# Performance work log

Hardware: AMD Instinct MI355X
Metric: run time of the kernel (lower is better)

The kernel has to match this reference:

```python
import jax, jax.numpy as jnp
import numpy as np

N6 = 100000
N8 = 100000
E = 400000
D = 128


def setup_inputs() -> dict:
    key = jax.random.key(0)
    ks = jax.random.split(key, 12)
    def msg(k):
        return jax.random.normal(k, (E, D), dtype=jnp.float32)
    def W(k):
        return jax.random.normal(k, (D, D), dtype=jnp.float32) / np.sqrt(D)
    def ei(k, n):
        return jax.random.randint(k, (E, 2), 0, n, dtype=jnp.int32)
    return {
        "msg_66": msg(ks[0]), "msg_68": msg(ks[1]),
        "msg_86": msg(ks[2]), "msg_88": msg(ks[3]),
        "W_66": W(ks[4]), "W_68": W(ks[5]), "W_86": W(ks[6]), "W_88": W(ks[7]),
        "ei_66": ei(ks[8], N6), "ei_68": ei(ks[9], N8),
        "ei_86": ei(ks[10], N6), "ei_88": ei(ks[11], N8),
        "num_nodes_6": N6, "num_nodes_8": N8,
    }


def _scatter_mean(v, dst, num_nodes):
    # torch_scatter reduce='mean': sum / count, count clamped to >=1 (zeros stay zero)
    s = jax.ops.segment_sum(v, dst, num_segments=num_nodes)
    c = jax.ops.segment_sum(jnp.ones((dst.shape[0],), v.dtype), dst, num_segments=num_nodes)
    return s / jnp.maximum(c, 1.0)[:, None]


def _proj_scatter(msg, W, ei, num_nodes):
    # per-edge-type linear (bias=False) then scatter-mean to dst nodes
    out = _scatter_mean(msg @ W, ei[:, 1], num_nodes)          # (num_nodes, D)
    # non-zero-row indicator (computed on detached values in the original)
    mask = jnp.any(jax.lax.stop_gradient(out) != 0, axis=-1).astype(out.dtype)  # (num_nodes,)
    return out, mask


def reference(msg_66, msg_68, msg_86, msg_88,
              W_66, W_68, W_86, W_88,
              ei_66, ei_68, ei_86, ei_88,
              num_nodes_6, num_nodes_8):
    # dict iteration order: "6-6", "6-8", "8-6", "8-8"; dst type is last token of key
    o66, m66 = _proj_scatter(msg_66, W_66, ei_66, num_nodes_6)
    o68, m68 = _proj_scatter(msg_68, W_68, ei_68, num_nodes_8)
    o86, m86 = _proj_scatter(msg_86, W_86, ei_86, num_nodes_6)
    o88, m88 = _proj_scatter(msg_88, W_88, ei_88, num_nodes_8)
    out_6 = jnp.stack([o66, o86], axis=1)   # (N6, num_edge_types_to_6=2, D)
    out_8 = jnp.stack([o68, o88], axis=1)   # (N8, 2, D)
    num_types_6 = m66 + m86                 # (N6,)
    num_types_8 = m68 + m88                 # (N8,)
    return out_6, out_8, num_types_6, num_types_8
```

## Files before the change

### kernel.cpp

```cpp
#include <hip/hip_runtime.h>

#define DF    128
#define EPB   1024
#define MAXB  512
#define TPB   64
#define ATS   132
#define WSTS  136
#define CAP   512

typedef __attribute__((ext_vector_type(8))) short short8;
typedef __attribute__((ext_vector_type(4))) float f32x4;

__device__ __forceinline__ unsigned short f2bf(float x) {
    unsigned u = __float_as_uint(x);
    u = (u + 0x7FFFu + ((u >> 16) & 1u)) >> 16;
    return (unsigned short)u;
}
__device__ __forceinline__ unsigned pack2bf(float a, float b) {
    return (unsigned)f2bf(a) | ((unsigned)f2bf(b) << 16);
}
__device__ __forceinline__ int rfl(int x) {
    return __builtin_amdgcn_readfirstlane(x);
}

struct AllParams {
    const float* msg[4];
    const float* Wm[4];
    float*       outp[4];
    int gb[4];
    int eb[4];
    int N[4];
    int cum[5];
};


__global__ void __launch_bounds__(256) count_kernel(
    const int* __restrict__ ei66, const int* __restrict__ ei86,
    const int* __restrict__ ei68, const int* __restrict__ ei88,
    int E66, int E86, int E68, int E88, int N6, int N8,
    int* __restrict__ base)
{
    int Etot = E66 + E86 + E68 + E88;
    for (int gid = blockIdx.x * 256 + threadIdx.x; gid < Etot;
         gid += gridDim.x * 256) {
        int le = gid, nb, dst;
        if (le < E66)               { dst = ei66[2 * le + 1]; nb = 0; }
        else if ((le -= E66) < E86) { dst = ei86[2 * le + 1]; nb = N6; }
        else if ((le -= E86) < E68) { dst = ei68[2 * le + 1]; nb = 2 * N6; }
        else { le -= E68;             dst = ei88[2 * le + 1]; nb = 2 * N6 + N8; }
        atomicAdd(base + nb + dst, 1);
    }
}

__global__ void __launch_bounds__(256) scan1_kernel(
    int* __restrict__ data, int M, int* __restrict__ bsum)
{
    __shared__ int ts[256];
    int t = threadIdx.x;
    int i0 = blockIdx.x * EPB + t * 4;
    int v0 = 0, v1 = 0, v2 = 0, v3 = 0;
    if (i0 + 3 < M) {
        int4 q = *(const int4*)(data + i0);
        v0 = q.x; v1 = q.y; v2 = q.z; v3 = q.w;
    } else {
        if (i0     < M) v0 = data[i0];
        if (i0 + 1 < M) v1 = data[i0 + 1];
        if (i0 + 2 < M) v2 = data[i0 + 2];
    }
    int sum = v0 + v1 + v2 + v3;
    ts[t] = sum;
    __syncthreads();
    for (int off = 1; off < 256; off <<= 1) {
        int x = (t >= off) ? ts[t - off] : 0;
        __syncthreads();
        ts[t] += x;
        __syncthreads();
    }
    int excl = ts[t] - sum;
    if (t == 255) bsum[blockIdx.x] = ts[255];
    int w0 = excl, w1 = excl + v0, w2 = w1 + v1, w3 = w2 + v2;
    if (i0 + 3 < M) {
        *(int4*)(data + i0) = make_int4(w0, w1, w2, w3);
    } else {
        if (i0     < M) data[i0]     = w0;
        if (i0 + 1 < M) data[i0 + 1] = w1;
        if (i0 + 2 < M) data[i0 + 2] = w2;
    }
}

__global__ void __launch_bounds__(256) scan2_kernel(int* __restrict__ bsum, int nb)
{
    __shared__ int s[MAXB];
    int t = threadIdx.x;
    s[t]       = (t       < nb) ? bsum[t]       : 0;
    s[t + 256] = (t + 256 < nb) ? bsum[t + 256] : 0;
    __syncthreads();
    int o0 = s[t], o1 = s[t + 256];
    for (int off = 1; off < MAXB; off <<= 1) {
        int a = (t       >= off) ? s[t       - off] : 0;
        int b = (t + 256 >= off) ? s[t + 256 - off] : 0;
        __syncthreads();
        s[t] += a; s[t + 256] += b;
        __syncthreads();
    }
    if (t       < nb) bsum[t]       = s[t]       - o0;
    if (t + 256 < nb) bsum[t + 256] = s[t + 256] - o1;
}

__global__ void __launch_bounds__(256) scan3_kernel(
    int* __restrict__ data, int M, const int* __restrict__ bsum)
{
    int add = bsum[blockIdx.x];
    if (add == 0) return;
    int i0 = blockIdx.x * EPB + threadIdx.x * 4;
    if (i0 + 3 < M) {
        int4 q = *(const int4*)(data + i0);
        q.x += add; q.y += add; q.z += add; q.w += add;
        *(int4*)(data + i0) = q;
    } else {
        if (i0     < M) data[i0]     += add;
        if (i0 + 1 < M) data[i0 + 1] += add;
        if (i0 + 2 < M) data[i0 + 2] += add;
    }
}

__global__ void __launch_bounds__(256) fill_kernel(
    const int* __restrict__ ei66, const int* __restrict__ ei86,
    const int* __restrict__ ei68, const int* __restrict__ ei88,
    int E66, int E86, int E68, int E88, int N6, int N8,
    int* __restrict__ base, int* __restrict__ csr)
{
    int Etot = E66 + E86 + E68 + E88;
    for (int gid = blockIdx.x * 256 + threadIdx.x; gid < Etot;
         gid += gridDim.x * 256) {
        int le = gid, nb, dst;
        if (le < E66)               { dst = ei66[2 * le + 1]; nb = 0; }
        else if ((le -= E66) < E86) { dst = ei86[2 * le + 1]; nb = N6; }
        else if ((le -= E86) < E68) { dst = ei68[2 * le + 1]; nb = 2 * N6; }
        else { le -= E68;             dst = ei88[2 * le + 1]; nb = 2 * N6 + N8; }
        int pos = atomicAdd(base + nb + dst, 1);
        csr[pos] = (int)((unsigned)gid | (((unsigned)(dst & 63)) << 26));
    }
}

__global__ void __launch_bounds__(256, 3) gather_mfma_kernel(
    const int* __restrict__ base, const int* __restrict__ csr, AllParams P)
{
    __shared__ alignas(16) short Wt[DF * WSTS];
    __shared__ alignas(16) short At[4][16 * ATS];
    __shared__ int eids[CAP];
    __shared__ int ends_s[TPB + 1];

    const int t    = threadIdx.x;
    const int lane = t & 63;
    const int w    = t >> 6;
    const int l15  = lane & 15;
    const int lg   = lane >> 4;
    short* Atw = At[w];

    int curty = -1;
    const int T = P.cum[4];

    for (int tt = blockIdx.x * 2; tt < blockIdx.x * 2 + 2 && tt < T; ++tt) {
        const int ty = (tt >= P.cum[2]) ? ((tt >= P.cum[3]) ? 3 : 2)
                                        : ((tt >= P.cum[1]) ? 1 : 0);
        const float* msg = P.msg[ty];
        const int gbase = P.gb[ty], ebase = P.eb[ty], N = P.N[ty];
        const int n0 = (tt - P.cum[ty]) * TPB;

        __syncthreads();

        if (ty != curty) {
            const float* Wm = P.Wm[ty];
            for (int idx = t; idx < 2048; idx += 256) {
                int k0 = (idx >> 5) << 1;
                int ng = (idx & 31) << 2;
                float4 wa = *(const float4*)(Wm + (size_t)k0 * DF + ng);
                float4 wb = *(const float4*)(Wm + (size_t)(k0 + 1) * DF + ng);
                float wav[4] = {wa.x, wa.y, wa.z, wa.w};
                float wbv[4] = {wb.x, wb.y, wb.z, wb.w};
                #pragma unroll
                for (int j = 0; j < 4; ++j)
                    *(unsigned*)(Wt + (ng + j) * WSTS + k0) =
                        pack2bf(wav[j], wbv[j]);
            }
            curty = ty;
        }

        if (t <= TPB) {
            int nn = n0 + t - 1;
            if (nn >= N) nn = N - 1;
            int gi = gbase + nn;
            ends_s[t] = (gi >= 0) ? base[gi] : 0;
        }
        {
            int gi0   = gbase + n0 - 1;
            int myts0 = (gi0 >= 0) ? base[gi0] : 0;
            int nn = n0 + TPB - 1; if (nn >= N) nn = N - 1;
            int myts1 = base[gbase + nn];
            int tot_all = myts1 - myts0;
            for (int i = t; i < tot_all && i < CAP; i += 256)
                eids[i] = csr[myts0 + i];
        }
        __syncthreads();

        const int ts0   = ends_s[0];
        const int wrow0 = w * 16;
        const int s0    = ends_s[wrow0];
        const int s1    = ends_s[wrow0 + 16];
        const int lbase = s0 - ts0;
        const int tot   = s1 - s0;
        int   cur = wrow0;
        float ax = 0.f, ay = 0.f;

#define LDE(eX, sb) { _Pragma("unroll")                                       \
        for (int j = 0; j < 8; ++j) {                                         \
            int ls = (sb) + j; ls = (ls < tot) ? ls : (tot - 1);              \
            int gs = lbase + ls;                                              \
            eX[j] = (gs < CAP) ? eids[gs] : csr[ts0 + gs]; } }

#define LDM(vX, eX) { _Pragma("unroll")                                       \
        for (int j = 0; j < 8; ++j) {                                         \
            int idx = (int)(((unsigned)eX[j]) & 0x03FFFFFFu) - ebase;         \
            vX[j] = *(const float2*)(msg + (size_t)idx * DF + 2 * lane); } }

#define FLUSHR() {                                                            \
        *(unsigned*)(Atw + (cur & 15) * ATS + 2 * lane) = pack2bf(ax, ay);    \
        ax = 0.f; ay = 0.f; ++cur; }

#define CONSB(vX, eX, sb) { _Pragma("unroll")                                 \
        for (int j = 0; j < 8; ++j) {                                         \
            if ((sb) + j < tot) {                                             \
                int rl = (int)(((unsigned)rfl(eX[j])) >> 26);                 \
                while (cur < rl) FLUSHR();                                    \
                ax += vX[j].x; ay += vX[j].y; } } }

        if (tot > 0) {
            int eA[8], eB[8], eC[8];
            float2 vA[8], vB[8], vC[8];
            const int nb = (tot + 7) >> 3;

            LDE(eA, 0); LDE(eB, 8);
            LDM(vA, eA); LDM(vB, eB);
            int ib = 0;
            while (true) {
                LDE(eC, ib * 8 + 16); LDM(vC, eC); CONSB(vA, eA, ib * 8);
                if (++ib >= nb) break;
                LDE(eA, ib * 8 + 16); LDM(vA, eA); CONSB(vB, eB, ib * 8);
                if (++ib >= nb) break;
                LDE(eB, ib * 8 + 16); LDM(vB, eB); CONSB(vC, eC, ib * 8);
                if (++ib >= nb) break;
            }
        }
        while (cur < wrow0 + 16) FLUSHR();
#undef LDE
#undef LDM
#undef FLUSHR
#undef CONSB

        f32x4 acc[8];
        #pragma unroll
        for (int j = 0; j < 8; ++j) acc[j] = (f32x4){0.f, 0.f, 0.f, 0.f};

        #pragma unroll
        for (int kk = 0; kk < 4; ++kk) {
            short8 av = *(const short8*)(Atw + l15 * ATS + kk * 32 + lg * 8);
            #pragma unroll
            for (int j = 0; j < 8; ++j) {
                short8 bv = *(const short8*)(Wt + (j * 16 + l15) * WSTS
                                             + kk * 32 + lg * 8);
                acc[j] = __builtin_amdgcn_mfma_f32_16x16x32_bf16(
                    av, bv, acc[j], 0, 0, 0);
            }
        }

        #pragma unroll
        for (int q = 0; q < 4; ++q) {
            int lrow = wrow0 + lg * 4 + q;
            int dg = ends_s[lrow + 1] - ends_s[lrow];
            float inv = (dg > 0) ? (1.0f / (float)dg) : 0.0f;
            #pragma unroll
            for (int j = 0; j < 8; ++j) acc[j][q] *= inv;
        }

        float* fA = (float*)Atw;
        float* outp = P.outp[ty];
        #pragma unroll
        for (int h = 0; h < 2; ++h) {
            if ((lg >> 1) == h) {
                int lr = (lg & 1) << 2;
                #pragma unroll
                for (int q = 0; q < 4; ++q)
                    #pragma unroll
                    for (int j = 0; j < 8; ++j)
                        fA[(lr + q) * DF + j * 16 + l15] = acc[j][q];
            }
            asm volatile("" ::: "memory");
            #pragma unroll
            for (int rr = 0; rr < 4; ++rr) {
                int lrh  = 2 * rr + (lane >> 5);
                int node = n0 + wrow0 + 8 * h + lrh;
                float4 x = *(const float4*)(fA + lrh * DF + (lane & 31) * 4);
                if (node < N)
                    *(float4*)(outp + (size_t)node * 256 + (lane & 31) * 4) = x;
            }
            asm volatile("" ::: "memory");
        }
    }
}

__global__ void __launch_bounds__(256) mask_kernel(
    const int* __restrict__ base, float* __restrict__ nt6,
    float* __restrict__ nt8, int N6, int N8)
{
    int i = blockIdx.x * blockDim.x + threadIdx.x;
    if (i < N6) {
        int g66 = i, g86 = N6 + i;
        int d66 = base[g66] - (g66 ? base[g66 - 1] : 0);
        int d86 = base[g86] - base[g86 - 1];
        nt6[i] = (float)((d66 > 0) + (d86 > 0));
    }
    if (i < N8) {
        int g68 = 2 * N6 + i, g88 = 2 * N6 + N8 + i;
        int d68 = base[g68] - base[g68 - 1];
        int d88 = base[g88] - base[g88 - 1];
        nt8[i] = (float)((d68 > 0) + (d88 > 0));
    }
}

extern "C" void kernel_launch(void* const* d_in, const int* in_sizes, int n_in,
                              void* d_out, int out_size, void* d_ws, size_t ws_size,
                              hipStream_t stream)
{
    const float* msg66 = (const float*)d_in[0];
    const float* msg68 = (const float*)d_in[1];
    const float* msg86 = (const float*)d_in[2];
    const float* msg88 = (const float*)d_in[3];
    const float* W66   = (const float*)d_in[4];
    const float* W68   = (const float*)d_in[5];
    const float* W86   = (const float*)d_in[6];
    const float* W88   = (const float*)d_in[7];
    const int*   ei66  = (const int*)d_in[8];
    const int*   ei68  = (const int*)d_in[9];
    const int*   ei86  = (const int*)d_in[10];
    const int*   ei88  = (const int*)d_in[11];

    int E66 = in_sizes[8]  / 2;
    int E68 = in_sizes[9]  / 2;
    int E86 = in_sizes[10] / 2;
    int E88 = in_sizes[11] / 2;
    int Etot = E66 + E86 + E68 + E88;

    size_t S  = (size_t)out_size / 257;
    int    N6 = (int)(S / 2);
    int    N8 = (int)(S - S / 2);
    int    M  = 2 * N6 + 2 * N8;

    float* out  = (float*)d_out;
    float* out6 = out;
    float* out8 = out + (size_t)N6 * 256;
    float* nt6  = out + (size_t)(N6 + N8) * 256;
    float* nt8  = nt6 + N6;

    int* base = (int*)d_ws;
    int* bsum = base + M;
    int* csr  = bsum + MAXB;

    int NB = (M + EPB - 1) / EPB;

    hipMemsetAsync(base, 0, (size_t)M * sizeof(int), stream);

    int eg = (Etot + 255) / 256;
    if (eg > 4096) eg = 4096;
    count_kernel<<<dim3(eg), dim3(256), 0, stream>>>(
        ei66, ei86, ei68, ei88, E66, E86, E68, E88, N6, N8, base);

    scan1_kernel<<<dim3(NB), dim3(256), 0, stream>>>(base, M, bsum);
    scan2_kernel<<<dim3(1),  dim3(256), 0, stream>>>(bsum, NB);
    scan3_kernel<<<dim3(NB), dim3(256), 0, stream>>>(base, M, bsum);

    fill_kernel<<<dim3(eg), dim3(256), 0, stream>>>(
        ei66, ei86, ei68, ei88, E66, E86, E68, E88, N6, N8, base, csr);

    int t6 = (N6 + TPB - 1) / TPB, t8 = (N8 + TPB - 1) / TPB;
    AllParams P;
    P.msg[0] = msg66; P.Wm[0] = W66; P.outp[0] = out6;       P.gb[0] = 0;           P.eb[0] = 0;                P.N[0] = N6;
    P.msg[1] = msg86; P.Wm[1] = W86; P.outp[1] = out6 + 128; P.gb[1] = N6;          P.eb[1] = E66;              P.N[1] = N6;
    P.msg[2] = msg68; P.Wm[2] = W68; P.outp[2] = out8;       P.gb[2] = 2 * N6;      P.eb[2] = E66 + E86;        P.N[2] = N8;
    P.msg[3] = msg88; P.Wm[3] = W88; P.outp[3] = out8 + 128; P.gb[3] = 2 * N6 + N8; P.eb[3] = E66 + E86 + E68;  P.N[3] = N8;
    P.cum[0] = 0;
    P.cum[1] = t6;
    P.cum[2] = 2 * t6;
    P.cum[3] = 2 * t6 + t8;
    P.cum[4] = 2 * t6 + 2 * t8;

    int G = (P.cum[4] + 1) / 2;
    gather_mfma_kernel<<<dim3(G), dim3(256), 0, stream>>>(base, csr, P);

    int Nmax = (N6 > N8) ? N6 : N8;
    mask_kernel<<<dim3((Nmax + 255) / 256), dim3(256), 0, stream>>>(
        base, nt6, nt8, N6, N8);
}
```

Before: 477.8 us.

## Swizzle LDS tiles with XOR layout and deepen gather prefetch pipeline

Replaces the padded LDS strides for the weight and aggregated-row tiles with an XOR-swizzled unpadded layout. This cuts bank conflicts on the short8 MFMA operand reads and the row flush writes, and slightly reduces LDS footprint. It also extends the message gather software pipeline from three to four in-flight 8-edge batches to hide more global load latency, at the cost of more registers under the 3-block occupancy bound. The row-index decode is now masked relative to wrow0.

```diff
diff --git a/kernel.cpp b/kernel.cpp
--- a/kernel.cpp
+++ b/kernel.cpp
@@ -4,8 +4,6 @@
 #define EPB   1024
 #define MAXB  512
 #define TPB   64
-#define ATS   132
-#define WSTS  136
 #define CAP   512
 
 typedef __attribute__((ext_vector_type(8))) short short8;
@@ -146,8 +144,8 @@
 __global__ void __launch_bounds__(256, 3) gather_mfma_kernel(
     const int* __restrict__ base, const int* __restrict__ csr, AllParams P)
 {
-    __shared__ alignas(16) short Wt[DF * WSTS];
-    __shared__ alignas(16) short At[4][16 * ATS];
+    __shared__ alignas(16) short Wt[DF * DF];
+    __shared__ alignas(16) short At[4][16 * DF];
     __shared__ int eids[CAP];
     __shared__ int ends_s[TPB + 1];
 
@@ -179,10 +177,14 @@
                 float4 wb = *(const float4*)(Wm + (size_t)(k0 + 1) * DF + ng);
                 float wav[4] = {wa.x, wa.y, wa.z, wa.w};
                 float wbv[4] = {wb.x, wb.y, wb.z, wb.w};
+                int cb = k0 >> 3, kl = k0 & 7;
                 #pragma unroll
-                for (int j = 0; j < 4; ++j)
-                    *(unsigned*)(Wt + (ng + j) * WSTS + k0) =
+                for (int j = 0; j < 4; ++j) {
+                    int n = ng + j;
+                    int chunk = cb ^ (n & 7);
+                    *(unsigned*)(Wt + n * DF + chunk * 8 + kl) =
                         pack2bf(wav[j], wbv[j]);
+                }
             }
             curty = ty;
         }
@@ -225,30 +227,34 @@
             vX[j] = *(const float2*)(msg + (size_t)idx * DF + 2 * lane); } }
 
 #define FLUSHR() {                                                            \
-        *(unsigned*)(Atw + (cur & 15) * ATS + 2 * lane) = pack2bf(ax, ay);    \
+        int lr_ = cur & 15;                                                   \
+        *(unsigned*)(Atw + lr_ * DF + ((((lane >> 2) ^ (lr_ & 7))) << 3)      \
+                     + ((lane & 3) << 1)) = pack2bf(ax, ay);                  \
         ax = 0.f; ay = 0.f; ++cur; }
 
 #define CONSB(vX, eX, sb) { _Pragma("unroll")                                 \
         for (int j = 0; j < 8; ++j) {                                         \
             if ((sb) + j < tot) {                                             \
-                int rl = (int)(((unsigned)rfl(eX[j])) >> 26);                 \
+                int rl = wrow0 + (int)((((unsigned)rfl(eX[j])) >> 26) & 15u); \
                 while (cur < rl) FLUSHR();                                    \
                 ax += vX[j].x; ay += vX[j].y; } } }
 
         if (tot > 0) {
-            int eA[8], eB[8], eC[8];
-            float2 vA[8], vB[8], vC[8];
+            int eA[8], eB[8], eC[8], eD[8];
+            float2 vA[8], vB[8], vC[8], vD[8];
             const int nb = (tot + 7) >> 3;
 
-            LDE(eA, 0); LDE(eB, 8);
-            LDM(vA, eA); LDM(vB, eB);
+            LDE(eA, 0); LDE(eB, 8); LDE(eC, 16);
+            LDM(vA, eA); LDM(vB, eB); LDM(vC, eC);
             int ib = 0;
             while (true) {
-                LDE(eC, ib * 8 + 16); LDM(vC, eC); CONSB(vA, eA, ib * 8);
+                LDE(eD, ib * 8 + 24); LDM(vD, eD); CONSB(vA, eA, ib * 8);
                 if (++ib >= nb) break;
-                LDE(eA, ib * 8 + 16); LDM(vA, eA); CONSB(vB, eB, ib * 8);
+                LDE(eA, ib * 8 + 24); LDM(vA, eA); CONSB(vB, eB, ib * 8);
                 if (++ib >= nb) break;
-                LDE(eB, ib * 8 + 16); LDM(vB, eB); CONSB(vC, eC, ib * 8);
+                LDE(eB, ib * 8 + 24); LDM(vB, eB); CONSB(vC, eC, ib * 8);
+                if (++ib >= nb) break;
+                LDE(eC, ib * 8 + 24); LDM(vC, eC); CONSB(vD, eD, ib * 8);
                 if (++ib >= nb) break;
             }
         }
@@ -264,11 +270,13 @@
 
         #pragma unroll
         for (int kk = 0; kk < 4; ++kk) {
-            short8 av = *(const short8*)(Atw + l15 * ATS + kk * 32 + lg * 8);
+            int c = kk * 4 + lg;
+            short8 av = *(const short8*)(Atw + l15 * DF
+                                         + ((c ^ (l15 & 7)) << 3));
             #pragma unroll
             for (int j = 0; j < 8; ++j) {
-                short8 bv = *(const short8*)(Wt + (j * 16 + l15) * WSTS
-                                             + kk * 32 + lg * 8);
+                int n = j * 16 + l15;
+                short8 bv = *(const short8*)(Wt + n * DF + ((c ^ (n & 7)) << 3));
                 acc[j] = __builtin_amdgcn_mfma_f32_16x16x32_bf16(
                     av, bv, acc[j], 0, 0, 0);
             }
```

After: 458.7 us. 4.0% less time.
